# Optimization experiments

Hardware: AMD Instinct MI355X
Metric: run time of the kernel (lower is better)

Reference implementation:

```python
import jax, jax.numpy as jnp
import numpy as np

HEAD_SIZE = 128
D_MODEL = 1024


def setup_inputs() -> dict:
    key = jax.random.key(0)
    kx, kq, kk, kv = jax.random.split(key, 4)
    B, T, C = 8, 2048, D_MODEL
    scale = 1.0 / np.sqrt(C)
    x = jax.random.normal(kx, (B, T, C), dtype=jnp.float32)
    # Dense(head_size, use_bias=False) weights, shape [C, head_size]
    Wq = jax.random.normal(kq, (C, HEAD_SIZE), dtype=jnp.float32) * scale
    Wk = jax.random.normal(kk, (C, HEAD_SIZE), dtype=jnp.float32) * scale
    Wv = jax.random.normal(kv, (C, HEAD_SIZE), dtype=jnp.float32) * scale
    return {"x": x, "Wq": Wq, "Wk": Wk, "Wv": Wv}


def reference(x, Wq, Wk, Wv):
    B, T, C = x.shape
    q = jnp.einsum('btc,ch->bth', x, Wq)  # [B,T,H]
    k = jnp.einsum('btc,ch->bth', x, Wk)
    v = jnp.einsum('btc,ch->bth', x, Wv)
    # NOTE: original scales by C**-0.5 (input channels), not head_size**-0.5
    scale = jnp.asarray(C, x.dtype) ** -0.5
    wei = jnp.einsum('bqh,bkh->bqk', q, k) * scale  # [B,T,T]
    causal = jnp.tril(jnp.ones((T, T), dtype=bool))
    wei = jnp.where(causal, wei, -jnp.inf)
    wei = jax.nn.softmax(wei, axis=-1)
    # dropout is identity in inference mode
    out = jnp.einsum('bqk,bkh->bqh', wei, v)  # [B,T,H]
    return out
```

## Files before the change

kernel.cpp:

```cpp
#include <hip/hip_runtime.h>

#define HS 128
#define DM 1024
#define BB 8
#define TT 2048

typedef __bf16 bf16;
typedef __bf16 bf16x8 __attribute__((ext_vector_type(8)));
typedef float f32x4 __attribute__((ext_vector_type(4)));

#define MFMA16(a, b, c) __builtin_amdgcn_mfma_f32_16x16x32_bf16(a, b, c, 0, 0, 0)
#define RAW_BARRIER() asm volatile("s_barrier" ::: "memory")

__device__ __forceinline__ void gll16(const bf16* g, bf16* l) {
  __builtin_amdgcn_global_load_lds(
      (const __attribute__((address_space(1))) void*)g,
      (__attribute__((address_space(3))) void*)l, 16, 0, 0);
}
__device__ __forceinline__ void gll16f(const float* g, float* l) {
  __builtin_amdgcn_global_load_lds(
      (const __attribute__((address_space(1))) void*)g,
      (__attribute__((address_space(3))) void*)l, 16, 0, 0);
}

__global__ __launch_bounds__(256) void wt_kernel(const float* __restrict__ Wq,
                                                 const float* __restrict__ Wk,
                                                 const float* __restrict__ Wv,
                                                 bf16* __restrict__ Wt) {
  __shared__ bf16 lt[128][72];
  const int mat = blockIdx.y;
  const float* W = mat == 0 ? Wq : (mat == 1 ? Wk : Wv);
  const int k0 = blockIdx.x * 64;
  const int t = threadIdx.x;
  for (int i = 0; i < 32; ++i) {
    int idx = t + i * 256;
    int k = idx >> 7;
    int h = idx & 127;
    lt[h][k] = (bf16)W[(size_t)(k0 + k) * HS + h];
  }
  __syncthreads();
  int h = t >> 1, half = t & 1;
  const uint4* src = (const uint4*)&lt[h][half * 32];
  uint4* dst = (uint4*)(Wt + ((size_t)mat * 128 + h) * DM + k0 + half * 32);
  dst[0] = src[0]; dst[1] = src[1]; dst[2] = src[2]; dst[3] = src[3];
}

__global__ __launch_bounds__(256) void qkv_kernel(const float* __restrict__ x,
                                                  const bf16* __restrict__ Wt,
                                                  bf16* __restrict__ Q,
                                                  bf16* __restrict__ K,
                                                  bf16* __restrict__ V) {
  __shared__ __align__(16) float xsf[2][2048];
  __shared__ __align__(16) bf16 wsb[2][12288];
  const int t = threadIdx.x, w = t >> 6, lane = t & 63, rl = lane & 15, quad = lane >> 4;
  const int row0 = blockIdx.x * 64;
  f32x4 acc[4][6] = {};

  auto stage = [&](int kt, int bufi) {
#pragma unroll
    for (int i2 = 0; i2 < 2; ++i2) {
      int s = w * 2 + i2;
      int row = s * 8 + (lane >> 3);
      int ch = (lane & 7) ^ (row & 7);
      gll16f(x + (size_t)(row0 + row) * DM + kt * 32 + ch * 4, &xsf[bufi][s * 256]);
    }
#pragma unroll
    for (int i2 = 0; i2 < 6; ++i2) {
      int s = w * 6 + i2;
      int row = s * 16 + (lane >> 2);
      int g = ((lane & 3) - (row >> 1)) & 3;
      gll16(Wt + (size_t)row * DM + kt * 32 + g * 8, &wsb[bufi][s * 512]);
    }
  };

  stage(0, 0);
  stage(1, 1);
  for (int kt = 0; kt < 32; ++kt) {
    const int cur = kt & 1;
    if (kt < 31) asm volatile("s_waitcnt vmcnt(8)" ::: "memory");
    else         asm volatile("s_waitcnt vmcnt(0)" ::: "memory");
    RAW_BARRIER();
    bf16x8 a[4];
#pragma unroll
    for (int rf = 0; rf < 4; ++rf) {
      int ar = rf * 16 + rl;
      int c0 = quad * 2;
      float4 f0 = *(const float4*)&xsf[cur][ar * 32 + ((c0 ^ (ar & 7)) << 2)];
      float4 f1 = *(const float4*)&xsf[cur][ar * 32 + (((c0 + 1) ^ (ar & 7)) << 2)];
      bf16x8 tv;
      tv[0] = (bf16)f0.x; tv[1] = (bf16)f0.y; tv[2] = (bf16)f0.z; tv[3] = (bf16)f0.w;
      tv[4] = (bf16)f1.x; tv[5] = (bf16)f1.y; tv[6] = (bf16)f1.z; tv[7] = (bf16)f1.w;
      a[rf] = tv;
    }
#pragma unroll
    for (int cf = 0; cf < 6; ++cf) {
      int br = w * 96 + cf * 16 + rl;
      bf16x8 bb = *(const bf16x8*)&wsb[cur][br * 32 + (((quad + (br >> 1)) & 3) << 3)];
#pragma unroll
      for (int rf = 0; rf < 4; ++rf) acc[rf][cf] = MFMA16(a[rf], bb, acc[rf][cf]);
    }
    RAW_BARRIER();
    if (kt < 30) stage(kt + 2, cur);
  }
#pragma unroll
  for (int cf = 0; cf < 6; ++cf) {
    int cg = w * 96 + cf * 16 + rl;
    int mat = cg >> 7, hcol = cg & 127;
    bf16* dst = mat == 0 ? Q : (mat == 1 ? K : V);
#pragma unroll
    for (int rf = 0; rf < 4; ++rf)
#pragma unroll
      for (int r = 0; r < 4; ++r) {
        int tg = row0 + rf * 16 + quad * 4 + r;
        dst[((size_t)tg << 7) + hcol] = (bf16)acc[rf][cf][r];
      }
  }
}

__global__ __launch_bounds__(256) void vtrans(const bf16* __restrict__ V,
                                              bf16* __restrict__ Vt) {
  __shared__ __align__(16) bf16 lt[4096];
  const int t = threadIdx.x;
  const int tt = blockIdx.x >> 1, hb = blockIdx.x & 1;
  const int t0 = tt * 64, h0 = hb * 64;
  const int r = t >> 2, seg = t & 3;
  bf16x8 a = *(const bf16x8*)(V + (size_t)(t0 + r) * HS + h0 + seg * 16);
  bf16x8 b2 = *(const bf16x8*)(V + (size_t)(t0 + r) * HS + h0 + seg * 16 + 8);
#pragma unroll
  for (int e = 0; e < 8; ++e) {
    int h = seg * 16 + e;
    lt[h * 64 + (((r >> 3) ^ (h & 7)) << 3) + (r & 7)] = a[e];
  }
#pragma unroll
  for (int e = 0; e < 8; ++e) {
    int h = seg * 16 + 8 + e;
    lt[h * 64 + (((r >> 3) ^ (h & 7)) << 3) + (r & 7)] = b2[e];
  }
  __syncthreads();
  const int hr = t >> 2, sg = t & 3;
  bf16x8 o0 = *(const bf16x8*)(lt + hr * 64 + (((sg * 2) ^ (hr & 7)) << 3));
  bf16x8 o1 = *(const bf16x8*)(lt + hr * 64 + (((sg * 2 + 1) ^ (hr & 7)) << 3));
  const int bidx = t0 >> 11, tt0 = t0 & 2047;
  bf16* dst = Vt + ((size_t)(bidx * 128 + h0 + hr) << 11) + tt0 + sg * 16;
  *(bf16x8*)dst = o0;
  *(bf16x8*)(dst + 8) = o1;
}

__global__ __launch_bounds__(256) void attn_kernel(const bf16* __restrict__ Qb,
                                                   const bf16* __restrict__ Kb,
                                                   const bf16* __restrict__ Vtb,
                                                   float* __restrict__ out) {
  __shared__ __align__(16) char smem[79104];
  bf16* qs = (bf16*)smem;
  bf16* ks = (bf16*)(smem + 8192);
  bf16* vt = (bf16*)(smem + 40960);
  float* Of = (float*)smem;
  float* ml = (float*)(smem + 78848);
  const int t = threadIdx.x, w = t >> 6, lane = t & 63, rl = lane & 15, quad = lane >> 4;
  const int wrow = w >> 1, kh = w & 1;
  const int rank = blockIdx.x >> 3, b = blockIdx.x & 7;
  const int qi = 63 - rank;
  const int q0 = qi * 32;
  const size_t base = (size_t)b * TT;
  const int KT = (qi >> 1) + 1;

#pragma unroll
  for (int i2 = 0; i2 < 2; ++i2) {
    int s = w * 2 + i2;
    int row = s * 4 + (lane >> 4);
    int ch = (lane & 15) ^ (row & 15);
    gll16(Qb + ((base + q0 + row) << 7) + ch * 8, qs + s * 512);
  }
  auto stageKV = [&](int slot) {
    int kt = min(slot, KT - 1);
    int bufi = slot & 1;
    bf16* ksb = ks + bufi * 8192;
    bf16* vtb = vt + bufi * 8192;
#pragma unroll
    for (int i2 = 0; i2 < 4; ++i2) {
      int s = w * 4 + i2;
      int rowk = s * 4 + (lane >> 4);
      int chk = (lane & 15) ^ (rowk & 15);
      gll16(Kb + ((base + kt * 64 + rowk) << 7) + chk * 8, ksb + s * 512);
      int rowv = s * 8 + (lane >> 3);
      int chv = (lane & 7) ^ (rowv & 7);
      gll16(Vtb + ((size_t)(b * 128 + rowv) << 11) + kt * 64 + chv * 8, vtb + s * 512);
    }
  };
  stageKV(0);
  stageKV(1);

  f32x4 o[8] = {};
  float lrow[4] = {0.f, 0.f, 0.f, 0.f};
  bf16* psw = (bf16*)(smem + 73728) + w * 640;

  for (int i = 0; i < KT; ++i) {
    const int cur = i & 1;
    asm volatile("s_waitcnt vmcnt(8)" ::: "memory");
    RAW_BARRIER();
    bf16* ksb = ks + cur * 8192;
    bf16* vtb = vt + cur * 8192;
    f32x4 s4[2] = {};
#pragma unroll
    for (int hc = 0; hc < 4; ++hc) {
      int arow = wrow * 16 + rl;
      bf16x8 a = *(const bf16x8*)(qs + arow * 128 + ((((hc << 2) + quad) ^ (arow & 15)) << 3));
#pragma unroll
      for (int c = 0; c < 2; ++c) {
        int brow = (kh * 2 + c) * 16 + rl;
        bf16x8 bb = *(const bf16x8*)(ksb + brow * 128 + ((((hc << 2) + quad) ^ (brow & 15)) << 3));
        s4[c] = MFMA16(a, bb, s4[c]);
      }
    }
    const bool diag = (i == KT - 1);
#pragma unroll
    for (int r = 0; r < 4; ++r) {
      int rloc = quad * 4 + r;
      int rowg = q0 + wrow * 16 + rloc;
      float psum = 0.f;
#pragma unroll
      for (int c = 0; c < 2; ++c) {
        int colg = i * 64 + kh * 32 + c * 16 + rl;
        float p = (diag && colg > rowg) ? 0.f : __expf(s4[c][r] * 0.03125f - 6.0f);
        psum += p;
        psw[rloc * 40 + c * 16 + rl] = (bf16)p;
      }
      lrow[r] += psum;
    }
    bf16x8 pa = *(const bf16x8*)(psw + rl * 40 + quad * 8);
#pragma unroll
    for (int ht = 0; ht < 8; ++ht) {
      int brow = ht * 16 + rl;
      bf16x8 bb = *(const bf16x8*)(vtb + brow * 64 + ((((kh << 2) + quad) ^ (brow & 7)) << 3));
      o[ht] = MFMA16(pa, bb, o[ht]);
    }
    RAW_BARRIER();
    if (i + 2 <= KT) stageKV(i + 2);
  }

#pragma unroll
  for (int r = 0; r < 4; ++r)
#pragma unroll
    for (int off = 1; off < 16; off <<= 1) lrow[r] += __shfl_xor(lrow[r], off, 64);
  __syncthreads();
#pragma unroll
  for (int ht = 0; ht < 8; ++ht)
#pragma unroll
    for (int r = 0; r < 4; ++r)
      Of[kh * 4096 + (wrow * 16 + quad * 4 + r) * 128 + ht * 16 + rl] = o[ht][r];
  if (rl == 0)
#pragma unroll
    for (int r = 0; r < 4; ++r) ml[kh * 32 + wrow * 16 + quad * 4 + r] = lrow[r];
  __syncthreads();
#pragma unroll
  for (int r = 0; r < 4; ++r) {
    int rowl = wrow * 16 + quad * 4 + r;
    float inv = 1.f / (ml[rowl] + ml[32 + rowl]);
#pragma unroll
    for (int hh = 0; hh < 4; ++hh) {
      int col = kh * 64 + hh * 16 + rl;
      out[((base + q0 + rowl) << 7) + col] =
          (Of[rowl * 128 + col] + Of[4096 + rowl * 128 + col]) * inv;
    }
  }
}

extern "C" void kernel_launch(void* const* d_in, const int* in_sizes, int n_in,
                              void* d_out, int out_size, void* d_ws, size_t ws_size,
                              hipStream_t stream) {
  const float* x = (const float*)d_in[0];
  const float* Wq = (const float*)d_in[1];
  const float* Wk = (const float*)d_in[2];
  const float* Wv = (const float*)d_in[3];
  float* out = (float*)d_out;
  char* ws = (char*)d_ws;
  bf16* Wt = (bf16*)ws;
  bf16* Q = (bf16*)(ws + 786432);
  bf16* K = (bf16*)(ws + 786432 + 4194304);
  bf16* V = (bf16*)(ws + 786432 + 2 * 4194304);
  bf16* Vt = (bf16*)(ws + 786432 + 3 * 4194304);
  wt_kernel<<<dim3(16, 3), 256, 0, stream>>>(Wq, Wk, Wv, Wt);
  qkv_kernel<<<dim3(256), 256, 0, stream>>>(x, Wt, Q, K, V);
  vtrans<<<dim3(512), 256, 0, stream>>>(V, Vt);
  attn_kernel<<<dim3(512), 256, 0, stream>>>(Q, K, Vt, out);
}
```

Measured before the change: 177.2 us.

## Split QKV projection across two column-half blocks with deeper K tiles

The QKV projection kernel now launches 512 blocks instead of 256, with each block computing 192 of the 384 output columns for 64 rows. Warps form a 2x2 grid over rows and columns. The K tile grows from 32 to 64, which halves the number of loop iterations and barriers, and the LDS swizzle is changed to match. The intent is to fill more of the MI355X compute units. The cost is that each block now loads the x tile twice and uses more LDS per block, which may limit occupancy.

```diff
diff --git a/kernel.cpp b/kernel.cpp
--- a/kernel.cpp
+++ b/kernel.cpp
@@ -50,68 +50,74 @@
                                                   bf16* __restrict__ Q,
                                                   bf16* __restrict__ K,
                                                   bf16* __restrict__ V) {
-  __shared__ __align__(16) float xsf[2][2048];
+  __shared__ __align__(16) float xsf[2][4096];
   __shared__ __align__(16) bf16 wsb[2][12288];
   const int t = threadIdx.x, w = t >> 6, lane = t & 63, rl = lane & 15, quad = lane >> 4;
-  const int row0 = blockIdx.x * 64;
-  f32x4 acc[4][6] = {};
+  const int rt = blockIdx.x >> 1, nb = blockIdx.x & 1;
+  const int row0 = rt * 64;
+  const int rw = w & 1, cw = w >> 1;
+  f32x4 acc[2][6] = {};
 
   auto stage = [&](int kt, int bufi) {
 #pragma unroll
-    for (int i2 = 0; i2 < 2; ++i2) {
-      int s = w * 2 + i2;
-      int row = s * 8 + (lane >> 3);
-      int ch = (lane & 7) ^ (row & 7);
-      gll16f(x + (size_t)(row0 + row) * DM + kt * 32 + ch * 4, &xsf[bufi][s * 256]);
+    for (int i2 = 0; i2 < 4; ++i2) {
+      int s = w * 4 + i2;
+      int row = s * 4 + (lane >> 4);
+      int cg = (lane & 15) ^ (row & 15);
+      gll16f(x + (size_t)(row0 + row) * DM + kt * 64 + cg * 4, &xsf[bufi][s * 256]);
     }
 #pragma unroll
     for (int i2 = 0; i2 < 6; ++i2) {
       int s = w * 6 + i2;
-      int row = s * 16 + (lane >> 2);
-      int g = ((lane & 3) - (row >> 1)) & 3;
-      gll16(Wt + (size_t)row * DM + kt * 32 + g * 8, &wsb[bufi][s * 512]);
+      int row = s * 8 + (lane >> 3);
+      int cg = (lane & 7) ^ (row & 7);
+      gll16(Wt + (size_t)(nb * 192 + row) * DM + kt * 64 + cg * 8, &wsb[bufi][s * 512]);
     }
   };
 
   stage(0, 0);
   stage(1, 1);
-  for (int kt = 0; kt < 32; ++kt) {
+  for (int kt = 0; kt < 16; ++kt) {
     const int cur = kt & 1;
-    if (kt < 31) asm volatile("s_waitcnt vmcnt(8)" ::: "memory");
+    if (kt < 15) asm volatile("s_waitcnt vmcnt(10)" ::: "memory");
     else         asm volatile("s_waitcnt vmcnt(0)" ::: "memory");
     RAW_BARRIER();
-    bf16x8 a[4];
-#pragma unroll
-    for (int rf = 0; rf < 4; ++rf) {
-      int ar = rf * 16 + rl;
-      int c0 = quad * 2;
-      float4 f0 = *(const float4*)&xsf[cur][ar * 32 + ((c0 ^ (ar & 7)) << 2)];
-      float4 f1 = *(const float4*)&xsf[cur][ar * 32 + (((c0 + 1) ^ (ar & 7)) << 2)];
-      bf16x8 tv;
-      tv[0] = (bf16)f0.x; tv[1] = (bf16)f0.y; tv[2] = (bf16)f0.z; tv[3] = (bf16)f0.w;
-      tv[4] = (bf16)f1.x; tv[5] = (bf16)f1.y; tv[6] = (bf16)f1.z; tv[7] = (bf16)f1.w;
-      a[rf] = tv;
-    }
-#pragma unroll
-    for (int cf = 0; cf < 6; ++cf) {
-      int br = w * 96 + cf * 16 + rl;
-      bf16x8 bb = *(const bf16x8*)&wsb[cur][br * 32 + (((quad + (br >> 1)) & 3) << 3)];
-#pragma unroll
-      for (int rf = 0; rf < 4; ++rf) acc[rf][cf] = MFMA16(a[rf], bb, acc[rf][cf]);
-    }
-    RAW_BARRIER();
-    if (kt < 30) stage(kt + 2, cur);
+#pragma unroll
+    for (int kc = 0; kc < 2; ++kc) {
+      bf16x8 a[2];
+#pragma unroll
+      for (int rf = 0; rf < 2; ++rf) {
+        int ar = rw * 32 + rf * 16 + rl;
+        int c0 = kc * 8 + quad * 2;
+        float4 f0 = *(const float4*)&xsf[cur][ar * 64 + (((c0) ^ (ar & 15)) << 2)];
+        float4 f1 = *(const float4*)&xsf[cur][ar * 64 + (((c0 + 1) ^ (ar & 15)) << 2)];
+        bf16x8 tv;
+        tv[0] = (bf16)f0.x; tv[1] = (bf16)f0.y; tv[2] = (bf16)f0.z; tv[3] = (bf16)f0.w;
+        tv[4] = (bf16)f1.x; tv[5] = (bf16)f1.y; tv[6] = (bf16)f1.z; tv[7] = (bf16)f1.w;
+        a[rf] = tv;
+      }
+#pragma unroll
+      for (int cf = 0; cf < 6; ++cf) {
+        int br = cw * 96 + cf * 16 + rl;
+        int cb = kc * 4 + quad;
+        bf16x8 bb = *(const bf16x8*)&wsb[cur][br * 64 + ((cb ^ (br & 7)) << 3)];
+        acc[0][cf] = MFMA16(a[0], bb, acc[0][cf]);
+        acc[1][cf] = MFMA16(a[1], bb, acc[1][cf]);
+      }
+    }
+    RAW_BARRIER();
+    if (kt < 14) stage(kt + 2, cur);
   }
 #pragma unroll
   for (int cf = 0; cf < 6; ++cf) {
-    int cg = w * 96 + cf * 16 + rl;
+    int cg = nb * 192 + cw * 96 + cf * 16 + rl;
     int mat = cg >> 7, hcol = cg & 127;
     bf16* dst = mat == 0 ? Q : (mat == 1 ? K : V);
 #pragma unroll
-    for (int rf = 0; rf < 4; ++rf)
+    for (int rf = 0; rf < 2; ++rf)
 #pragma unroll
       for (int r = 0; r < 4; ++r) {
-        int tg = row0 + rf * 16 + quad * 4 + r;
+        int tg = row0 + rw * 32 + rf * 16 + quad * 4 + r;
         dst[((size_t)tg << 7) + hcol] = (bf16)acc[rf][cf][r];
       }
   }
@@ -280,7 +286,7 @@
   bf16* V = (bf16*)(ws + 786432 + 2 * 4194304);
   bf16* Vt = (bf16*)(ws + 786432 + 3 * 4194304);
   wt_kernel<<<dim3(16, 3), 256, 0, stream>>>(Wq, Wk, Wv, Wt);
-  qkv_kernel<<<dim3(256), 256, 0, stream>>>(x, Wt, Q, K, V);
+  qkv_kernel<<<dim3(512), 256, 0, stream>>>(x, Wt, Q, K, V);
   vtrans<<<dim3(512), 256, 0, stream>>>(V, Vt);
   attn_kernel<<<dim3(512), 256, 0, stream>>>(Q, K, Vt, out);
 }
```

New measurement: 154.0 us. 1.15x faster.
